# Performance work log

Hardware: AMD Instinct MI355X
Metric: run time of the kernel (lower is better)

The kernel has to match this reference:

```python
import jax, jax.numpy as jnp
import numpy as np

N = 50000   # num nodes
E = 800000  # num edges
D_IN, D_HID, D_OUT = 128, 128, 64


def setup_inputs() -> dict:
    key = jax.random.key(0)
    ks = jax.random.split(key, 10)
    x = jax.random.normal(ks[0], (N, D_IN), dtype=jnp.float32)
    edge_index = jax.random.randint(ks[1], (2, E), 0, N, dtype=jnp.int32)
    edge_weight = jax.random.uniform(ks[2], (E,), dtype=jnp.float32)
    def lin(k, fan_in, fan_out):
        bound = 1.0 / np.sqrt(fan_in)
        kw, kb = jax.random.split(k)
        W = jax.random.uniform(kw, (fan_out, fan_in), minval=-bound, maxval=bound, dtype=jnp.float32)
        b = jax.random.uniform(kb, (fan_out,), minval=-bound, maxval=bound, dtype=jnp.float32)
        return W, b
    W0, b0 = lin(ks[3], 2 * D_IN, D_HID)
    W1, b1 = lin(ks[4], 2 * D_HID, D_HID)
    W2, b2 = lin(ks[5], 2 * D_HID, D_OUT)
    return {"x": x, "edge_index": edge_index, "edge_weight": edge_weight,
            "W0": W0, "b0": b0, "W1": W1, "b1": b1, "W2": W2, "b2": b2}


def _sage_layer(x, row, col, ew, W, b):
    # weighted mean aggregation over incoming edges (dst = row, src = col)
    n = x.shape[0]
    msg = x[col] * ew[:, None]                      # [E, D] gather + scale
    agg = jax.ops.segment_sum(msg, row, num_segments=n)    # [N, D]
    deg = jax.ops.segment_sum(ew, row, num_segments=n)     # [N]
    deg = jnp.clip(deg, 1.0, None)[:, None]
    h = jnp.concatenate([x, agg / deg], axis=-1)    # [N, 2D]
    return h @ W.T + b


def reference(x, edge_index, edge_weight, W0, b0, W1, b1, W2, b2):
    row, col = edge_index[0], edge_index[1]
    h = jax.nn.relu(_sage_layer(x, row, col, edge_weight, W0, b0))
    h = jax.nn.relu(_sage_layer(h, row, col, edge_weight, W1, b1))
    return _sage_layer(h, row, col, edge_weight, W2, b2)
```

## Files before the change

### kernel.cpp

```cpp
#include <hip/hip_runtime.h>


#define D 128
#define K2 256
#define NQ 4
#define QW 12500

typedef __attribute__((ext_vector_type(8))) short short8;
typedef __attribute__((ext_vector_type(4))) float floatx4;

__device__ inline unsigned short rne_bf16(float f) {
    unsigned int u = __float_as_uint(f);
    u += 0x7fffu + ((u >> 16) & 1u);
    return (unsigned short)(u >> 16);
}

__device__ inline int quarter_of(int c) {
    return (c >= 2 * QW) ? ((c >= 3 * QW) ? 3 : 2) : ((c >= QW) ? 1 : 0);
}

__global__ void prep_kernel(const float* __restrict__ x, unsigned short* __restrict__ x_hi,
                            const float* __restrict__ W0, const float* __restrict__ W1,
                            const float* __restrict__ W2,
                            unsigned short* __restrict__ h0, unsigned short* __restrict__ l0,
                            unsigned short* __restrict__ h1, unsigned short* __restrict__ l1,
                            unsigned short* __restrict__ h2, unsigned short* __restrict__ l2,
                            const int* __restrict__ row, const int* __restrict__ col,
                            int* __restrict__ cnt, int n4, int E) {
    int b = blockIdx.x;
    int tid = threadIdx.x;
    if (b < 6250) {
        int i = b * 256 + tid;
        if (i < n4) {
            float4 v = reinterpret_cast<const float4*>(x)[i];
            ushort4 o;
            o.x = rne_bf16(v.x); o.y = rne_bf16(v.y); o.z = rne_bf16(v.z); o.w = rne_bf16(v.w);
            reinterpret_cast<ushort4*>(x_hi)[i] = o;
        }
    } else if (b < 6570) {
        int i = (b - 6250) * 256 + tid;
        const float* w; unsigned short *hi, *lo; int sidx, didx;
        if (i < 32768)      { w = W0; hi = h0; lo = l0; sidx = i; didx = i; }
        else if (i < 65536) { w = W1; hi = h1; lo = l1; sidx = i - 32768; didx = sidx; }
        else if (i < 81920) {
            w = W2; hi = h2; lo = l2;
            int i2 = i - 65536;
            int r = i2 >> 7, k = i2 & 127;
            sidx = (r < 64) ? (r * 256 + k) : ((r - 64) * 256 + 128 + k);
            didx = i2;
        }
        else return;
        float f = w[sidx];
        unsigned short h = rne_bf16(f);
        float fh = __uint_as_float(((unsigned int)h) << 16);
        hi[didx] = h;
        lo[didx] = rne_bf16(f - fh);
    } else {
        int e = (b - 6570) * 256 + tid;
        if (e < E) {
            int key = row[e] * NQ + quarter_of(col[e]);
            atomicAdd(&cnt[key], 1);
        }
    }
}

__global__ void scan1_kernel(const int* __restrict__ cnt, int* __restrict__ rowptr,
                             int* __restrict__ bsum, int NB) {
    __shared__ int s[256];
    int tid = threadIdx.x;
    int gid = blockIdx.x * 256 + tid;
    int v = (gid < NB) ? cnt[gid] : 0;
    s[tid] = v;
    __syncthreads();
    for (int off = 1; off < 256; off <<= 1) {
        int t = (tid >= off) ? s[tid - off] : 0;
        __syncthreads();
        s[tid] += t;
        __syncthreads();
    }
    if (gid < NB) rowptr[gid] = s[tid] - v;
    if (tid == 255) bsum[blockIdx.x] = s[255];
}

__global__ void scan2_kernel(int* __restrict__ bsum, int* __restrict__ boff, int nb) {
    __shared__ int s[1024];
    int tid = threadIdx.x;
    int v = (tid < nb) ? bsum[tid] : 0;
    s[tid] = v;
    __syncthreads();
    for (int off = 1; off < 1024; off <<= 1) {
        int t = (tid >= off) ? s[tid - off] : 0;
        __syncthreads();
        s[tid] += t;
        __syncthreads();
    }
    if (tid < nb) boff[tid] = s[tid] - v;
}

__global__ void scan3_kernel(int* __restrict__ rowptr, const int* __restrict__ boff,
                             int* __restrict__ cursor, int NB, int E) {
    int gid = blockIdx.x * 256 + threadIdx.x;
    if (gid < NB) {
        int v = rowptr[gid] + boff[gid >> 8];
        rowptr[gid] = v;
        cursor[gid] = v;
    } else if (gid == NB) {
        rowptr[NB] = E;
    }
}

__global__ void scatter_ranged(const int* __restrict__ row, const int* __restrict__ col,
                               const float* __restrict__ ew, int* __restrict__ cursor,
                               int2* __restrict__ ep, int E) {
    int b = blockIdx.x;
    int r = b & 7;
    int q = b >> 3;
    int nchunk = gridDim.x >> 3;
    int chunk = (E + nchunk - 1) / nchunk;
    int e0 = q * chunk;
    int e1 = e0 + chunk; if (e1 > E) e1 = E;
    int lo = r * 6250, hi = lo + 6250;
    for (int e = e0 + (int)threadIdx.x; e < e1; e += (int)blockDim.x) {
        int rw = row[e];
        if (rw >= lo && rw < hi) {
            int c = col[e];
            int key = rw * NQ + quarter_of(c);
            int p = atomicAdd(&cursor[key], 1);
            ep[p] = make_int2(c, __float_as_int(ew[e]));
        }
    }
}

__device__ inline void accum8(float* acc, uint4 a, float w) {
    acc[0] += __uint_as_float(a.x << 16) * w;
    acc[1] += __uint_as_float(a.x & 0xffff0000u) * w;
    acc[2] += __uint_as_float(a.y << 16) * w;
    acc[3] += __uint_as_float(a.y & 0xffff0000u) * w;
    acc[4] += __uint_as_float(a.z << 16) * w;
    acc[5] += __uint_as_float(a.z & 0xffff0000u) * w;
    acc[6] += __uint_as_float(a.w << 16) * w;
    acc[7] += __uint_as_float(a.w & 0xffff0000u) * w;
}

__global__ void gather_agg_bf(const unsigned short* __restrict__ src, const int* __restrict__ rowptr4,
                              const int2* __restrict__ ep, unsigned short* __restrict__ agg, int N) {
    long long t = (long long)blockIdx.x * blockDim.x + threadIdx.x;
    int wid = (int)(t >> 6);
    int lane = threadIdx.x & 63;
    int slot = lane >> 4;
    int fl = lane & 15;
    int n = wid * 4 + slot;
    if (n >= N) return;
    int beg = rowptr4[n * 4], end = rowptr4[n * 4 + 4];
    float acc[8];
#pragma unroll
    for (int j = 0; j < 8; j++) acc[j] = 0.f;
    float ds = 0.f;
    int e = beg;
    for (; e + 7 < end; e += 8) {
        int2 p[8];
#pragma unroll
        for (int u = 0; u < 8; u++) p[u] = ep[e + u];
        uint4 a[8];
#pragma unroll
        for (int u = 0; u < 8; u++)
            a[u] = *reinterpret_cast<const uint4*>(src + (size_t)p[u].x * D + fl * 8);
#pragma unroll
        for (int u = 0; u < 8; u++) {
            float w = __int_as_float(p[u].y);
            accum8(acc, a[u], w);
            ds += w;
        }
    }
    for (; e + 3 < end; e += 4) {
        int2 p[4];
#pragma unroll
        for (int u = 0; u < 4; u++) p[u] = ep[e + u];
#pragma unroll
        for (int u = 0; u < 4; u++) {
            uint4 a = *reinterpret_cast<const uint4*>(src + (size_t)p[u].x * D + fl * 8);
            float w = __int_as_float(p[u].y);
            accum8(acc, a, w);
            ds += w;
        }
    }
    for (; e < end; ++e) {
        int2 p = ep[e];
        uint4 a = *reinterpret_cast<const uint4*>(src + (size_t)p.x * D + fl * 8);
        float w = __int_as_float(p.y);
        accum8(acc, a, w);
        ds += w;
    }
    float inv = 1.0f / (ds > 1.f ? ds : 1.f);
    uint4 o;
    o.x = (unsigned int)rne_bf16(acc[0] * inv) | ((unsigned int)rne_bf16(acc[1] * inv) << 16);
    o.y = (unsigned int)rne_bf16(acc[2] * inv) | ((unsigned int)rne_bf16(acc[3] * inv) << 16);
    o.z = (unsigned int)rne_bf16(acc[4] * inv) | ((unsigned int)rne_bf16(acc[5] * inv) << 16);
    o.w = (unsigned int)rne_bf16(acc[6] * inv) | ((unsigned int)rne_bf16(acc[7] * inv) << 16);
    *reinterpret_cast<uint4*>(agg + (size_t)n * D + fl * 8) = o;
}

template<bool RELU, bool BF16OUT, int OSTRIDE>
__global__ __launch_bounds__(256) void sage_gemm(
    const unsigned short* __restrict__ src, const unsigned short* __restrict__ agg,
    const unsigned short* __restrict__ Whi, const unsigned short* __restrict__ Wlo,
    const float* __restrict__ bias, float* __restrict__ outf,
    unsigned short* __restrict__ outb, int N) {
    __shared__ short sW[2][32][260];
    int tid = threadIdx.x;
    int c0 = blockIdx.y * 32;

    for (int i = tid; i < 2048; i += 256) {
        int h = i >> 10;
        int rem = i & 1023;
        int r = rem & 31;
        int k8 = rem >> 5;
        const unsigned short* wp = (h ? Wlo : Whi) + (size_t)(c0 + r) * K2 + k8 * 8;
        *reinterpret_cast<uint4*>(&sW[h][r][k8 * 8]) = *reinterpret_cast<const uint4*>(wp);
    }
    __syncthreads();

    int lane = tid & 63;
    int wv = tid >> 6;
    int nlane = lane & 15;
    int quad = lane >> 4;
    int m0 = blockIdx.x * 128 + wv * 32;
    int r0 = m0 + nlane;      if (r0 >= N) r0 = N - 1;
    int r1 = m0 + 16 + nlane; if (r1 >= N) r1 = N - 1;

    short8 a[2][8];
#pragma unroll
    for (int ks = 0; ks < 8; ks++) {
        int k0 = ks * 32;
        const unsigned short* p0 = (k0 < D) ? (src + (size_t)r0 * D + k0)
                                            : (agg + (size_t)r0 * D + (k0 - D));
        const unsigned short* p1 = (k0 < D) ? (src + (size_t)r1 * D + k0)
                                            : (agg + (size_t)r1 * D + (k0 - D));
        a[0][ks] = *reinterpret_cast<const short8*>(p0 + quad * 8);
        a[1][ks] = *reinterpret_cast<const short8*>(p1 + quad * 8);
    }

    floatx4 acc[2][2];
#pragma unroll
    for (int mt = 0; mt < 2; mt++)
#pragma unroll
        for (int nt = 0; nt < 2; nt++) acc[mt][nt] = (floatx4){0.f, 0.f, 0.f, 0.f};

#pragma unroll
    for (int ks = 0; ks < 8; ks++) {
        int k0 = ks * 32;
#pragma unroll
        for (int nt = 0; nt < 2; nt++) {
            short8 bh = *reinterpret_cast<const short8*>(&sW[0][nt * 16 + nlane][k0 + quad * 8]);
            short8 bl = *reinterpret_cast<const short8*>(&sW[1][nt * 16 + nlane][k0 + quad * 8]);
            acc[0][nt] = __builtin_amdgcn_mfma_f32_16x16x32_bf16(a[0][ks], bh, acc[0][nt], 0, 0, 0);
            acc[0][nt] = __builtin_amdgcn_mfma_f32_16x16x32_bf16(a[0][ks], bl, acc[0][nt], 0, 0, 0);
            acc[1][nt] = __builtin_amdgcn_mfma_f32_16x16x32_bf16(a[1][ks], bh, acc[1][nt], 0, 0, 0);
            acc[1][nt] = __builtin_amdgcn_mfma_f32_16x16x32_bf16(a[1][ks], bl, acc[1][nt], 0, 0, 0);
        }
    }

#pragma unroll
    for (int nt = 0; nt < 2; nt++) {
        int c = c0 + nt * 16 + nlane;
        float bb = bias[c];
#pragma unroll
        for (int mt = 0; mt < 2; mt++) {
#pragma unroll
            for (int r = 0; r < 4; r++) {
                int node = m0 + mt * 16 + quad * 4 + r;
                if (node < N) {
                    float y = acc[mt][nt][r] + bb;
                    if (RELU) y = y > 0.f ? y : 0.f;
                    if (BF16OUT) outb[(size_t)node * OSTRIDE + c] = rne_bf16(y);
                    else         outf[(size_t)node * OSTRIDE + c] = y;
                }
            }
        }
    }
}

__global__ __launch_bounds__(256) void sage_gemm2(
    const unsigned short* __restrict__ h1, const unsigned short* __restrict__ Whi,
    const unsigned short* __restrict__ Wlo, const float* __restrict__ b2,
    float* __restrict__ ytop2, unsigned short* __restrict__ z2, int N) {
    __shared__ short sW[2][32][132];
    int tid = threadIdx.x;
    int c0 = blockIdx.y * 32;

    for (int i = tid; i < 1024; i += 256) {
        int h = i >> 9;
        int rem = i & 511;
        int r = rem & 31;
        int k8 = rem >> 5;
        const unsigned short* wp = (h ? Wlo : Whi) + (size_t)(c0 + r) * 128 + k8 * 8;
        *reinterpret_cast<uint4*>(&sW[h][r][k8 * 8]) = *reinterpret_cast<const uint4*>(wp);
    }
    __syncthreads();

    int lane = tid & 63;
    int wv = tid >> 6;
    int nlane = lane & 15;
    int quad = lane >> 4;
    int m0 = blockIdx.x * 128 + wv * 32;
    int r0 = m0 + nlane;      if (r0 >= N) r0 = N - 1;
    int r1 = m0 + 16 + nlane; if (r1 >= N) r1 = N - 1;

    short8 a[2][4];
#pragma unroll
    for (int ks = 0; ks < 4; ks++) {
        a[0][ks] = *reinterpret_cast<const short8*>(h1 + (size_t)r0 * D + ks * 32 + quad * 8);
        a[1][ks] = *reinterpret_cast<const short8*>(h1 + (size_t)r1 * D + ks * 32 + quad * 8);
    }

    floatx4 acc[2][2];
#pragma unroll
    for (int mt = 0; mt < 2; mt++)
#pragma unroll
        for (int nt = 0; nt < 2; nt++) acc[mt][nt] = (floatx4){0.f, 0.f, 0.f, 0.f};

#pragma unroll
    for (int ks = 0; ks < 4; ks++) {
        int k0 = ks * 32;
#pragma unroll
        for (int nt = 0; nt < 2; nt++) {
            short8 bh = *reinterpret_cast<const short8*>(&sW[0][nt * 16 + nlane][k0 + quad * 8]);
            short8 bl = *reinterpret_cast<const short8*>(&sW[1][nt * 16 + nlane][k0 + quad * 8]);
            acc[0][nt] = __builtin_amdgcn_mfma_f32_16x16x32_bf16(a[0][ks], bh, acc[0][nt], 0, 0, 0);
            acc[0][nt] = __builtin_amdgcn_mfma_f32_16x16x32_bf16(a[0][ks], bl, acc[0][nt], 0, 0, 0);
            acc[1][nt] = __builtin_amdgcn_mfma_f32_16x16x32_bf16(a[1][ks], bh, acc[1][nt], 0, 0, 0);
            acc[1][nt] = __builtin_amdgcn_mfma_f32_16x16x32_bf16(a[1][ks], bl, acc[1][nt], 0, 0, 0);
        }
    }

#pragma unroll
    for (int nt = 0; nt < 2; nt++) {
        int c = c0 + nt * 16 + nlane;
#pragma unroll
        for (int mt = 0; mt < 2; mt++) {
#pragma unroll
            for (int r = 0; r < 4; r++) {
                int node = m0 + mt * 16 + quad * 4 + r;
                if (node < N) {
                    float v = acc[mt][nt][r];
                    if (c < 64) ytop2[(size_t)node * 64 + c] = v + b2[c];
                    else        z2[(size_t)node * 64 + (c - 64)] = rne_bf16(v);
                }
            }
        }
    }
}

__global__ void gather_out(const unsigned short* __restrict__ z2, const int* __restrict__ rowptr4,
                           const int2* __restrict__ ep, const float* __restrict__ ytop2,
                           float* __restrict__ out, int N) {
    long long t = (long long)blockIdx.x * blockDim.x + threadIdx.x;
    int wid = (int)(t >> 6);
    int lane = threadIdx.x & 63;
    int slot = lane >> 3;
    int fl = lane & 7;
    int n = wid * 8 + slot;
    if (n >= N) return;
    int beg = rowptr4[n * 4], end = rowptr4[n * 4 + 4];
    float acc[8];
#pragma unroll
    for (int j = 0; j < 8; j++) acc[j] = 0.f;
    float ds = 0.f;
    int e = beg;
    for (; e + 7 < end; e += 8) {
        int2 p[8];
#pragma unroll
        for (int u = 0; u < 8; u++) p[u] = ep[e + u];
        uint4 a[8];
#pragma unroll
        for (int u = 0; u < 8; u++)
            a[u] = *reinterpret_cast<const uint4*>(z2 + (size_t)p[u].x * 64 + fl * 8);
#pragma unroll
        for (int u = 0; u < 8; u++) {
            float w = __int_as_float(p[u].y);
            accum8(acc, a[u], w);
            ds += w;
        }
    }
    for (; e < end; ++e) {
        int2 p = ep[e];
        uint4 a = *reinterpret_cast<const uint4*>(z2 + (size_t)p.x * 64 + fl * 8);
        float w = __int_as_float(p.y);
        accum8(acc, a, w);
        ds += w;
    }
    float inv = 1.0f / (ds > 1.f ? ds : 1.f);
    const float* yt = ytop2 + (size_t)n * 64 + fl * 8;
    float* op = out + (size_t)n * 64 + fl * 8;
    float4 t0 = *reinterpret_cast<const float4*>(yt);
    float4 t1 = *reinterpret_cast<const float4*>(yt + 4);
    float4 o0 = make_float4(t0.x + acc[0] * inv, t0.y + acc[1] * inv,
                            t0.z + acc[2] * inv, t0.w + acc[3] * inv);
    float4 o1 = make_float4(t1.x + acc[4] * inv, t1.y + acc[5] * inv,
                            t1.z + acc[6] * inv, t1.w + acc[7] * inv);
    *reinterpret_cast<float4*>(op) = o0;
    *reinterpret_cast<float4*>(op + 4) = o1;
}

extern "C" void kernel_launch(void* const* d_in, const int* in_sizes, int n_in,
                              void* d_out, int out_size, void* d_ws, size_t ws_size,
                              hipStream_t stream) {
    const float* x  = (const float*)d_in[0];
    const int*   ei = (const int*)d_in[1];
    const float* ew = (const float*)d_in[2];
    const float* W0 = (const float*)d_in[3];
    const float* b0 = (const float*)d_in[4];
    const float* W1 = (const float*)d_in[5];
    const float* b1 = (const float*)d_in[6];
    const float* W2 = (const float*)d_in[7];
    const float* b2 = (const float*)d_in[8];
    float* out = (float*)d_out;

    const int N = 50000;
    const int E = in_sizes[2];
    const int NB = N * NQ;
    const int* row = ei;
    const int* col = ei + E;

    char* base = (char*)d_ws;
    size_t ND = (size_t)N * D;
    unsigned short* x_hi   = (unsigned short*)base;               base += ND * 2;
    unsigned short* h0_hi  = (unsigned short*)base;               base += ND * 2;
    unsigned short* h1_hi  = (unsigned short*)base;               base += ND * 2;
    unsigned short* agg_hi = (unsigned short*)base;               base += ND * 2;
    int2* ep               = (int2*)base;                         base += (size_t)E * 8;
    int* rowptr4           = (int*)base;                          base += (size_t)(NB + 1) * 4;
    unsigned short* W0hi   = (unsigned short*)base;               base += 128 * 256 * 2;
    unsigned short* W0lo   = (unsigned short*)base;               base += 128 * 256 * 2;
    unsigned short* W1hi   = (unsigned short*)base;               base += 128 * 256 * 2;
    unsigned short* W1lo   = (unsigned short*)base;               base += 128 * 256 * 2;
    unsigned short* W2Chi  = (unsigned short*)base;               base += 128 * 128 * 2;
    unsigned short* W2Clo  = (unsigned short*)base;               base += 128 * 128 * 2;

    int* cnt    = (int*)h0_hi;
    int* cursor = cnt + NB;
    int* bsum   = cursor + NB;
    int* boff   = bsum + 1024;

    float* ytop2          = (float*)agg_hi;
    unsigned short* z2    = (unsigned short*)h0_hi;

    int nbScan = (NB + 255) / 256;

    hipMemsetAsync(cnt, 0, (size_t)NB * sizeof(int), stream);
    int n4 = (int)(ND / 4);
    prep_kernel<<<9695, 256, 0, stream>>>(x, x_hi, W0, W1, W2,
        W0hi, W0lo, W1hi, W1lo, W2Chi, W2Clo, row, col, cnt, n4, E);

    scan1_kernel<<<nbScan, 256, 0, stream>>>(cnt, rowptr4, bsum, NB);
    scan2_kernel<<<1, 1024, 0, stream>>>(bsum, boff, nbScan);
    scan3_kernel<<<(NB + 256) / 256 + 1, 256, 0, stream>>>(rowptr4, boff, cursor, NB, E);
    scatter_ranged<<<2048, 256, 0, stream>>>(row, col, ew, cursor, ep, E);

    int nWaves = (N + 3) / 4;
    int aggBlocks = (int)(((long long)nWaves * 64 + 255) / 256);
    int nodeTiles = (N + 127) / 128;
    dim3 g128(nodeTiles, 4);

    gather_agg_bf<<<aggBlocks, 256, 0, stream>>>(x_hi, rowptr4, ep, agg_hi, N);
    sage_gemm<true, true, D><<<g128, 256, 0, stream>>>(
        x_hi, agg_hi, W0hi, W0lo, b0, nullptr, h0_hi, N);

    gather_agg_bf<<<aggBlocks, 256, 0, stream>>>(h0_hi, rowptr4, ep, agg_hi, N);
    sage_gemm<true, true, D><<<g128, 256, 0, stream>>>(
        h0_hi, agg_hi, W1hi, W1lo, b1, nullptr, h1_hi, N);

    sage_gemm2<<<g128, 256, 0, stream>>>(h1_hi, W2Chi, W2Clo, b2, ytop2, z2, N);
    int nWaves2 = (N + 7) / 8;
    int outBlocks = (int)(((long long)nWaves2 * 64 + 255) / 256);
    gather_out<<<outBlocks, 256, 0, stream>>>(z2, rowptr4, ep, ytop2, out, N);
}
```

Before: 325.2 us.

## Replace global-atomic CSR scatter with per-range LDS cursors and byte range tags

Prep now writes a byte tag per edge giving its destination row range (196 rows each). A new scatter kernel gives each of 256 blocks one row range: it scans the tag array, queues matching edge ids in LDS, and fills ep using LDS-resident cursors seeded from rowptr, with no global atomics. This removes global atomic contention and the cursor array, but every block re-reads the full E-byte tag array, and queue overflow falls back to slower direct processing.

Result: slower. 391.8 us (+20.5%).

```diff
diff --git a/kernel.cpp b/kernel.cpp
--- a/kernel.cpp
+++ b/kernel.cpp
@@ -5,6 +5,10 @@
 #define K2 256
 #define NQ 4
 #define QW 12500
+#define NRANGE 256
+#define RROWS 196
+#define RBINS (RROWS * NQ)
+#define QCAP 6144
 
 typedef __attribute__((ext_vector_type(8))) short short8;
 typedef __attribute__((ext_vector_type(4))) float floatx4;
@@ -26,7 +30,8 @@
                             unsigned short* __restrict__ h1, unsigned short* __restrict__ l1,
                             unsigned short* __restrict__ h2, unsigned short* __restrict__ l2,
                             const int* __restrict__ row, const int* __restrict__ col,
-                            int* __restrict__ cnt, int n4, int E) {
+                            int* __restrict__ cnt, unsigned char* __restrict__ rbArr,
+                            int n4, int E) {
     int b = blockIdx.x;
     int tid = threadIdx.x;
     if (b < 6250) {
@@ -58,8 +63,10 @@
     } else {
         int e = (b - 6570) * 256 + tid;
         if (e < E) {
-            int key = row[e] * NQ + quarter_of(col[e]);
+            int rw = row[e];
+            int key = rw * NQ + quarter_of(col[e]);
             atomicAdd(&cnt[key], 1);
+            rbArr[e] = (unsigned char)(rw / RROWS);
         }
     }
 }
@@ -98,36 +105,79 @@
 }
 
 __global__ void scan3_kernel(int* __restrict__ rowptr, const int* __restrict__ boff,
-                             int* __restrict__ cursor, int NB, int E) {
+                             int NB, int E) {
     int gid = blockIdx.x * 256 + threadIdx.x;
     if (gid < NB) {
-        int v = rowptr[gid] + boff[gid >> 8];
-        rowptr[gid] = v;
-        cursor[gid] = v;
+        rowptr[gid] = rowptr[gid] + boff[gid >> 8];
     } else if (gid == NB) {
         rowptr[NB] = E;
     }
 }
 
-__global__ void scatter_ranged(const int* __restrict__ row, const int* __restrict__ col,
-                               const float* __restrict__ ew, int* __restrict__ cursor,
-                               int2* __restrict__ ep, int E) {
+__global__ __launch_bounds__(512) void scatter_lds(
+    const unsigned char* __restrict__ rb, const int* __restrict__ row,
+    const int* __restrict__ col, const float* __restrict__ ew,
+    const int* __restrict__ rowptr4, int2* __restrict__ ep, int E, int NB) {
+    __shared__ int cur[RBINS];
+    __shared__ int q[QCAP];
+    __shared__ int qn;
     int b = blockIdx.x;
-    int r = b & 7;
-    int q = b >> 3;
-    int nchunk = gridDim.x >> 3;
-    int chunk = (E + nchunk - 1) / nchunk;
-    int e0 = q * chunk;
-    int e1 = e0 + chunk; if (e1 > E) e1 = E;
-    int lo = r * 6250, hi = lo + 6250;
-    for (int e = e0 + (int)threadIdx.x; e < e1; e += (int)blockDim.x) {
-        int rw = row[e];
-        if (rw >= lo && rw < hi) {
-            int c = col[e];
-            int key = rw * NQ + quarter_of(c);
-            int p = atomicAdd(&cursor[key], 1);
-            ep[p] = make_int2(c, __float_as_int(ew[e]));
-        }
+    int tid = threadIdx.x;
+    int base = b * RBINS;
+    for (int i = tid; i < RBINS; i += 512) {
+        int g = base + i;
+        cur[i] = (g < NB) ? rowptr4[g] : 0;
+    }
+    if (tid == 0) qn = 0;
+    __syncthreads();
+
+    unsigned int bb = (unsigned int)b;
+    int nv = E >> 4;
+    const uint4* rb4 = reinterpret_cast<const uint4*>(rb);
+    for (int v = tid; v < nv; v += 512) {
+        uint4 o = rb4[v];
+        unsigned int wd[4] = {o.x, o.y, o.z, o.w};
+#pragma unroll
+        for (int j = 0; j < 4; j++) {
+#pragma unroll
+            for (int k = 0; k < 4; k++) {
+                if (((wd[j] >> (k * 8)) & 255u) == bb) {
+                    int e = v * 16 + j * 4 + k;
+                    int idx = atomicAdd(&qn, 1);
+                    if (idx < QCAP) {
+                        q[idx] = e;
+                    } else {
+                        int c = col[e];
+                        int key = row[e] * NQ + quarter_of(c);
+                        int p = atomicAdd(&cur[key - base], 1);
+                        ep[p] = make_int2(c, __float_as_int(ew[e]));
+                    }
+                }
+            }
+        }
+    }
+    for (int e = (nv << 4) + tid; e < E; e += 512) {
+        if (rb[e] == (unsigned char)b) {
+            int idx = atomicAdd(&qn, 1);
+            if (idx < QCAP) {
+                q[idx] = e;
+            } else {
+                int c = col[e];
+                int key = row[e] * NQ + quarter_of(c);
+                int p = atomicAdd(&cur[key - base], 1);
+                ep[p] = make_int2(c, __float_as_int(ew[e]));
+            }
+        }
+    }
+    __syncthreads();
+
+    int m = qn < QCAP ? qn : QCAP;
+    for (int i = tid; i < m; i += 512) {
+        int e = q[i];
+        int c = col[e];
+        int key = row[e] * NQ + quarter_of(c);
+        int p = atomicAdd(&cur[key - base], 1);
+        ep[p] = make_int2(c, __float_as_int(ew[e]));
     }
 }
 
@@ -436,11 +486,12 @@
     unsigned short* W1lo   = (unsigned short*)base;               base += 128 * 256 * 2;
     unsigned short* W2Chi  = (unsigned short*)base;               base += 128 * 128 * 2;
     unsigned short* W2Clo  = (unsigned short*)base;               base += 128 * 128 * 2;
-
-    int* cnt    = (int*)h0_hi;
-    int* cursor = cnt + NB;
-    int* bsum   = cursor + NB;
-    int* boff   = bsum + 1024;
+    base = (char*)(((uintptr_t)base + 15) & ~(uintptr_t)15);
+    unsigned char* rbArr   = (unsigned char*)base;                base += (size_t)E + 16;
+
+    int* cnt  = (int*)h0_hi;
+    int* bsum = cnt + NB;
+    int* boff = bsum + 1024;
 
     float* ytop2          = (float*)agg_hi;
     unsigned short* z2    = (unsigned short*)h0_hi;
@@ -450,12 +501,12 @@
     hipMemsetAsync(cnt, 0, (size_t)NB * sizeof(int), stream);
     int n4 = (int)(ND / 4);
     prep_kernel<<<9695, 256, 0, stream>>>(x, x_hi, W0, W1, W2,
-        W0hi, W0lo, W1hi, W1lo, W2Chi, W2Clo, row, col, cnt, n4, E);
+        W0hi, W0lo, W1hi, W1lo, W2Chi, W2Clo, row, col, cnt, rbArr, n4, E);
 
     scan1_kernel<<<nbScan, 256, 0, stream>>>(cnt, rowptr4, bsum, NB);
     scan2_kernel<<<1, 1024, 0, stream>>>(bsum, boff, nbScan);
-    scan3_kernel<<<(NB + 256) / 256 + 1, 256, 0, stream>>>(rowptr4, boff, cursor, NB, E);
-    scatter_ranged<<<2048, 256, 0, stream>>>(row, col, ew, cursor, ep, E);
+    scan3_kernel<<<(NB + 256) / 256 + 1, 256, 0, stream>>>(rowptr4, boff, NB, E);
+    scatter_lds<<<NRANGE, 512, 0, stream>>>(rbArr, row, col, ew, rowptr4, ep, E, NB);
 
     int nWaves = (N + 3) / 4;
     int aggBlocks = (int)(((long long)nWaves * 64 + 255) / 256);
```
